# Kernel tuning notes

Hardware: AMD Instinct MI355X
Metric: run time of the kernel (lower is better)

## Reference

```python
import jax, jax.numpy as jnp
import numpy as np
from jax import lax

B, S, H = 8192, 64, 128
ODE_UNFOLDS = 4
EPSILON = 1e-8


def setup_inputs() -> dict:
    key = jax.random.key(0)
    ks = jax.random.split(key, 10)
    return {
        "input": jax.random.normal(ks[0], (B, S), jnp.float32),
        "hidden": jax.random.normal(ks[1], (B, H), jnp.float32),
        "sensory_mu": jax.random.normal(ks[2], (S, H), jnp.float32),
        "sensory_sigma": jax.random.uniform(ks[3], (S, H), jnp.float32, 1.0, 5.0),
        "sensory_W": jax.random.normal(ks[4], (S, H), jnp.float32) * 0.1,
        "hidden_mu": jax.random.normal(ks[5], (H, H), jnp.float32),
        "hidden_sigma": jax.random.uniform(ks[6], (H, H), jnp.float32, 1.0, 5.0),
        "hidden_W": jax.random.normal(ks[7], (H, H), jnp.float32) * 0.1,
        "w_tau": jax.random.uniform(ks[8], (H,), jnp.float32, 0.1, 1.0),
        "w_A": jax.random.normal(ks[9], (H,), jnp.float32),
        "elapsed_time": jnp.float32(1.0),
    }


def reference(input, hidden, sensory_mu, sensory_sigma, sensory_W,
              hidden_mu, hidden_sigma, hidden_W, w_tau, w_A, elapsed_time):
    # sensory_activation: per-synapse sigmoid gate summed over sensory dim -> [B, H]
    sens = jnp.einsum(
        "bsh,sh->bh",
        jax.nn.sigmoid(sensory_sigma * (input[:, :, None] - sensory_mu)),
        sensory_W,
    )
    dt = elapsed_time / ODE_UNFOLDS

    def step(state, _):
        # hidden_activation: sensory response + recurrent sigmoid-gated synapses -> [B, H]
        resp = sens + jnp.einsum(
            "bph,ph->bh",
            jax.nn.sigmoid(hidden_sigma * (state[:, :, None] - hidden_mu)),
            hidden_W,
        )
        numerator = state + dt * w_A * resp
        denominator = 1.0 + dt * w_tau + dt * resp
        return numerator / (denominator + EPSILON), None

    last_state, _ = lax.scan(step, hidden, None, length=ODE_UNFOLDS)
    return last_state
```

## Files before the change

kernel.cpp:

```cpp
#include <hip/hip_runtime.h>

#define BATCH   8192
#define SDIM    64
#define HDIM    128
#define NB      8
#define PAD     12
#define UNFOLDS 4

typedef float f32x2 __attribute__((ext_vector_type(2)));
typedef float f32x4 __attribute__((ext_vector_type(4)));

__device__ __forceinline__ void sig_acc(f32x4 P, f32x4 xv,
                                        f32x2& acc0, f32x2& acc1) {
    f32x2 av = {P.x, P.x}, cv = {P.y, P.y}, wv = {P.z, P.z};
    const f32x2 one = {1.0f, 1.0f};
    const f32x2 cap = {60.0f, 60.0f};
    f32x2 z0 = __builtin_elementwise_fma(xv.xy, av, cv);
    f32x2 z1 = __builtin_elementwise_fma(xv.zw, av, cv);
    z0 = __builtin_elementwise_min(z0, cap);
    z1 = __builtin_elementwise_min(z1, cap);
    f32x2 e0, e1;
    e0.x = __builtin_amdgcn_exp2f(z0.x);
    e0.y = __builtin_amdgcn_exp2f(z0.y);
    e1.x = __builtin_amdgcn_exp2f(z1.x);
    e1.y = __builtin_amdgcn_exp2f(z1.y);
    f32x2 d0 = e0 + one;
    f32x2 d1 = e1 + one;
    f32x2 Pp = d0 * d1;
    f32x2 rP;
    rP.x = __builtin_amdgcn_rcpf(Pp.x);
    rP.y = __builtin_amdgcn_rcpf(Pp.y);
    f32x2 t = wv * rP;
    acc0 = __builtin_elementwise_fma(t, d1, acc0);
    acc1 = __builtin_elementwise_fma(t, d0, acc1);
}

__global__ __launch_bounds__(256) void prep_kernel(
    const float* __restrict__ s_mu, const float* __restrict__ s_sig,
    const float* __restrict__ s_W,
    const float* __restrict__ h_mu, const float* __restrict__ h_sig,
    const float* __restrict__ h_W,
    f32x4* __restrict__ hpk, f32x4* __restrict__ spk)
{
    const float LOG2E = 1.4426950408889634f;
    int i = blockIdx.x * 256 + threadIdx.x;
    if (i < HDIM * HDIM) {
        float a = -LOG2E * h_sig[i];
        hpk[i] = (f32x4){a, -a * h_mu[i], h_W[i], 0.0f};
    }
    if (i < SDIM * HDIM) {
        float a = -LOG2E * s_sig[i];
        spk[i] = (f32x4){a, -a * s_mu[i], s_W[i], 0.0f};
    }
}

__global__ __launch_bounds__(256, 4) void ltc_main(
    const float* __restrict__ input,
    const float* __restrict__ hidden,
    const f32x4* __restrict__ spk,
    const f32x4* __restrict__ hpk,
    const float* __restrict__ w_tau,
    const float* __restrict__ w_A,
    const float* __restrict__ elapsed,
    float* __restrict__ out)
{
    const int tid = threadIdx.x;
    const int h   = tid & (HDIM - 1);
    const int g   = tid >> 7;
    const int b0  = blockIdx.x * NB;

    __shared__ float st [HDIM][PAD];
    __shared__ float xin[SDIM][PAD];

    for (int i = tid; i < NB * SDIM; i += 256) {
        int r = i >> 6, s = i & (SDIM - 1);
        xin[s][r] = input[(b0 + r) * SDIM + s];
    }
    for (int i = tid; i < NB * HDIM; i += 256) {
        int r = i >> 7, p = i & (HDIM - 1);
        st[p][r] = hidden[(b0 + r) * HDIM + p];
    }
    __syncthreads();

    const float dt = elapsed[0] * (1.0f / UNFOLDS);

#define LD4(arr, idx) (*(const f32x4*)&(arr)[idx][g * 4])

    f32x2 sens0 = {0.0f, 0.0f}, sens1 = {0.0f, 0.0f};
    #pragma unroll 8
    for (int s = 0; s < SDIM; ++s) {
        f32x4 P = spk[s * HDIM + h];
        f32x4 x = LD4(xin, s);
        sig_acc(P, x, sens0, sens1);
    }

    const float wT  = w_tau[h];
    const float wA  = w_A[h];
    const float dA  = dt * wA;
    const float dT1 = fmaf(dt, wT, 1.0f) + 1e-8f;
    const f32x2 dAv  = {dA, dA};
    const f32x2 dtv  = {dt, dt};
    const f32x2 dT1v = {dT1, dT1};

    f32x4 ns;

    for (int it = 0; it < UNFOLDS; ++it) {
        f32x2 acc0 = sens0, acc1 = sens1;

        #pragma unroll 8
        for (int p = 0; p < HDIM; ++p) {
            f32x4 P = hpk[p * HDIM + h];
            f32x4 x = LD4(st, p);
            sig_acc(P, x, acc0, acc1);
        }

        f32x4 old = LD4(st, h);
        f32x2 n0 = __builtin_elementwise_fma(dAv, acc0, old.xy);
        f32x2 n1 = __builtin_elementwise_fma(dAv, acc1, old.zw);
        f32x2 d0 = __builtin_elementwise_fma(dtv, acc0, dT1v);
        f32x2 d1 = __builtin_elementwise_fma(dtv, acc1, dT1v);
        ns.x = n0.x * __builtin_amdgcn_rcpf(d0.x);
        ns.y = n0.y * __builtin_amdgcn_rcpf(d0.y);
        ns.z = n1.x * __builtin_amdgcn_rcpf(d1.x);
        ns.w = n1.y * __builtin_amdgcn_rcpf(d1.y);

        __syncthreads();
        *(f32x4*)&st[h][g * 4] = ns;
        __syncthreads();
    }

    out[(b0 + g * 4 + 0) * HDIM + h] = ns.x;
    out[(b0 + g * 4 + 1) * HDIM + h] = ns.y;
    out[(b0 + g * 4 + 2) * HDIM + h] = ns.z;
    out[(b0 + g * 4 + 3) * HDIM + h] = ns.w;
}

extern "C" void kernel_launch(void* const* d_in, const int* in_sizes, int n_in,
                              void* d_out, int out_size, void* d_ws, size_t ws_size,
                              hipStream_t stream) {
    const float* input   = (const float*)d_in[0];
    const float* hidden  = (const float*)d_in[1];
    const float* s_mu    = (const float*)d_in[2];
    const float* s_sig   = (const float*)d_in[3];
    const float* s_W     = (const float*)d_in[4];
    const float* h_mu    = (const float*)d_in[5];
    const float* h_sig   = (const float*)d_in[6];
    const float* h_W     = (const float*)d_in[7];
    const float* w_tau   = (const float*)d_in[8];
    const float* w_A     = (const float*)d_in[9];
    const float* elapsed = (const float*)d_in[10];
    float* out = (float*)d_out;

    f32x4* hpk = (f32x4*)d_ws;
    f32x4* spk = hpk + HDIM * HDIM;

    prep_kernel<<<dim3((HDIM * HDIM + 255) / 256), dim3(256), 0, stream>>>(
        s_mu, s_sig, s_W, h_mu, h_sig, h_W, hpk, spk);

    ltc_main<<<dim3(BATCH / NB), dim3(256), 0, stream>>>(
        input, hidden, spk, hpk, w_tau, w_A, elapsed, out);
}
```

Before: 125.0 us.

## Process 16 batch rows per block and use per-element reciprocals in sigmoid

Doubles batch rows per block from 8 to 16, so each thread handles 8 rows and every packed parameter load from global memory feeds twice the sigmoid work. The sigmoid accumulation goes back to one reciprocal per element instead of a shared product reciprocal, and the exp clamp is dropped; this adds transcendental work but removes the multiplies. The launch-bounds occupancy hint is removed and the grid shrinks to 512 blocks, which may reduce latency hiding on a large GPU. Dropping the clamp is still safe, because an overflowing exp gives a reciprocal of zero, which is the correct sigmoid limit.

New measurement: 124.5 us. Within noise of the previous version (-0.4%).

```diff
diff --git a/kernel.cpp b/kernel.cpp
--- a/kernel.cpp
+++ b/kernel.cpp
@@ -3,8 +3,8 @@
 #define BATCH   8192
 #define SDIM    64
 #define HDIM    128
-#define NB      8
-#define PAD     12
+#define NB      16
+#define NBP     20
 #define UNFOLDS 4
 
 typedef float f32x2 __attribute__((ext_vector_type(2)));
@@ -14,11 +14,8 @@
                                         f32x2& acc0, f32x2& acc1) {
     f32x2 av = {P.x, P.x}, cv = {P.y, P.y}, wv = {P.z, P.z};
     const f32x2 one = {1.0f, 1.0f};
-    const f32x2 cap = {60.0f, 60.0f};
     f32x2 z0 = __builtin_elementwise_fma(xv.xy, av, cv);
     f32x2 z1 = __builtin_elementwise_fma(xv.zw, av, cv);
-    z0 = __builtin_elementwise_min(z0, cap);
-    z1 = __builtin_elementwise_min(z1, cap);
     f32x2 e0, e1;
     e0.x = __builtin_amdgcn_exp2f(z0.x);
     e0.y = __builtin_amdgcn_exp2f(z0.y);
@@ -26,13 +23,13 @@
     e1.y = __builtin_amdgcn_exp2f(z1.y);
     f32x2 d0 = e0 + one;
     f32x2 d1 = e1 + one;
-    f32x2 Pp = d0 * d1;
-    f32x2 rP;
-    rP.x = __builtin_amdgcn_rcpf(Pp.x);
-    rP.y = __builtin_amdgcn_rcpf(Pp.y);
-    f32x2 t = wv * rP;
-    acc0 = __builtin_elementwise_fma(t, d1, acc0);
-    acc1 = __builtin_elementwise_fma(t, d0, acc1);
+    f32x2 r0, r1;
+    r0.x = __builtin_amdgcn_rcpf(d0.x);
+    r0.y = __builtin_amdgcn_rcpf(d0.y);
+    r1.x = __builtin_amdgcn_rcpf(d1.x);
+    r1.y = __builtin_amdgcn_rcpf(d1.y);
+    acc0 = __builtin_elementwise_fma(wv, r0, acc0);
+    acc1 = __builtin_elementwise_fma(wv, r1, acc1);
 }
 
 __global__ __launch_bounds__(256) void prep_kernel(
@@ -54,7 +51,7 @@
     }
 }
 
-__global__ __launch_bounds__(256, 4) void ltc_main(
+__global__ __launch_bounds__(256) void ltc_main(
     const float* __restrict__ input,
     const float* __restrict__ hidden,
     const f32x4* __restrict__ spk,
@@ -69,8 +66,8 @@
     const int g   = tid >> 7;
     const int b0  = blockIdx.x * NB;
 
-    __shared__ float st [HDIM][PAD];
-    __shared__ float xin[SDIM][PAD];
+    __shared__ float st [HDIM][NBP];
+    __shared__ float xin[SDIM][NBP];
 
     for (int i = tid; i < NB * SDIM; i += 256) {
         int r = i >> 6, s = i & (SDIM - 1);
@@ -84,14 +81,18 @@
 
     const float dt = elapsed[0] * (1.0f / UNFOLDS);
 
-#define LD4(arr, idx) (*(const f32x4*)&(arr)[idx][g * 4])
+#define LD4A(arr, idx) (*(const f32x4*)&(arr)[idx][g * 8])
+#define LD4B(arr, idx) (*(const f32x4*)&(arr)[idx][g * 8 + 4])
 
-    f32x2 sens0 = {0.0f, 0.0f}, sens1 = {0.0f, 0.0f};
-    #pragma unroll 8
+    f32x2 sA0 = {0.0f, 0.0f}, sA1 = {0.0f, 0.0f};
+    f32x2 sB0 = {0.0f, 0.0f}, sB1 = {0.0f, 0.0f};
+    #pragma unroll 4
     for (int s = 0; s < SDIM; ++s) {
-        f32x4 P = spk[s * HDIM + h];
-        f32x4 x = LD4(xin, s);
-        sig_acc(P, x, sens0, sens1);
+        f32x4 P  = spk[s * HDIM + h];
+        f32x4 xa = LD4A(xin, s);
+        f32x4 xb = LD4B(xin, s);
+        sig_acc(P, xa, sA0, sA1);
+        sig_acc(P, xb, sB0, sB1);
     }
 
     const float wT  = w_tau[h];
@@ -102,37 +103,53 @@
     const f32x2 dtv  = {dt, dt};
     const f32x2 dT1v = {dT1, dT1};
 
-    f32x4 ns;
+    f32x4 nsA, nsB;
 
     for (int it = 0; it < UNFOLDS; ++it) {
-        f32x2 acc0 = sens0, acc1 = sens1;
+        f32x2 aA0 = sA0, aA1 = sA1, aB0 = sB0, aB1 = sB1;
 
-        #pragma unroll 8
+        #pragma unroll 4
         for (int p = 0; p < HDIM; ++p) {
-            f32x4 P = hpk[p * HDIM + h];
-            f32x4 x = LD4(st, p);
-            sig_acc(P, x, acc0, acc1);
+            f32x4 P  = hpk[p * HDIM + h];
+            f32x4 xa = LD4A(st, p);
+            f32x4 xb = LD4B(st, p);
+            sig_acc(P, xa, aA0, aA1);
+            sig_acc(P, xb, aB0, aB1);
         }
 
-        f32x4 old = LD4(st, h);
-        f32x2 n0 = __builtin_elementwise_fma(dAv, acc0, old.xy);
-        f32x2 n1 = __builtin_elementwise_fma(dAv, acc1, old.zw);
-        f32x2 d0 = __builtin_elementwise_fma(dtv, acc0, dT1v);
-        f32x2 d1 = __builtin_elementwise_fma(dtv, acc1, dT1v);
-        ns.x = n0.x * __builtin_amdgcn_rcpf(d0.x);
-        ns.y = n0.y * __builtin_amdgcn_rcpf(d0.y);
-        ns.z = n1.x * __builtin_amdgcn_rcpf(d1.x);
-        ns.w = n1.y * __builtin_amdgcn_rcpf(d1.y);
+        f32x4 oldA = LD4A(st, h);
+        f32x4 oldB = LD4B(st, h);
+        f32x2 nA0 = __builtin_elementwise_fma(dAv, aA0, oldA.xy);
+        f32x2 nA1 = __builtin_elementwise_fma(dAv, aA1, oldA.zw);
+        f32x2 nB0 = __builtin_elementwise_fma(dAv, aB0, oldB.xy);
+        f32x2 nB1 = __builtin_elementwise_fma(dAv, aB1, oldB.zw);
+        f32x2 dA0 = __builtin_elementwise_fma(dtv, aA0, dT1v);
+        f32x2 dA1 = __builtin_elementwise_fma(dtv, aA1, dT1v);
+        f32x2 dB0 = __builtin_elementwise_fma(dtv, aB0, dT1v);
+        f32x2 dB1 = __builtin_elementwise_fma(dtv, aB1, dT1v);
+        nsA.x = nA0.x * __builtin_amdgcn_rcpf(dA0.x);
+        nsA.y = nA0.y * __builtin_amdgcn_rcpf(dA0.y);
+        nsA.z = nA1.x * __builtin_amdgcn_rcpf(dA1.x);
+        nsA.w = nA1.y * __builtin_amdgcn_rcpf(dA1.y);
+        nsB.x = nB0.x * __builtin_amdgcn_rcpf(dB0.x);
+        nsB.y = nB0.y * __builtin_amdgcn_rcpf(dB0.y);
+        nsB.z = nB1.x * __builtin_amdgcn_rcpf(dB1.x);
+        nsB.w = nB1.y * __builtin_amdgcn_rcpf(dB1.y);
 
         __syncthreads();
-        *(f32x4*)&st[h][g * 4] = ns;
+        *(f32x4*)&st[h][g * 8]     = nsA;
+        *(f32x4*)&st[h][g * 8 + 4] = nsB;
         __syncthreads();
     }
 
-    out[(b0 + g * 4 + 0) * HDIM + h] = ns.x;
-    out[(b0 + g * 4 + 1) * HDIM + h] = ns.y;
-    out[(b0 + g * 4 + 2) * HDIM + h] = ns.z;
-    out[(b0 + g * 4 + 3) * HDIM + h] = ns.w;
+    out[(b0 + g * 8 + 0) * HDIM + h] = nsA.x;
+    out[(b0 + g * 8 + 1) * HDIM + h] = nsA.y;
+    out[(b0 + g * 8 + 2) * HDIM + h] = nsA.z;
+    out[(b0 + g * 8 + 3) * HDIM + h] = nsA.w;
+    out[(b0 + g * 8 + 4) * HDIM + h] = nsB.x;
+    out[(b0 + g * 8 + 5) * HDIM + h] = nsB.y;
+    out[(b0 + g * 8 + 6) * HDIM + h] = nsB.z;
+    out[(b0 + g * 8 + 7) * HDIM + h] = nsB.w;
 }
 
 extern "C" void kernel_launch(void* const* d_in, const int* in_sizes, int n_in,
```
